# Optimization experiments

Hardware: AMD Instinct MI355X
Metric: run time of the kernel (lower is better)

The kernel has to match this reference:

```python
import jax, jax.numpy as jnp
import numpy as np

UNITS = 256
IN_DIM = 256
OUT_DIM = 10
TOL = 1e-4
MAX_ITER = 50


def setup_inputs() -> dict:
    key = jax.random.key(0)
    ks = jax.random.split(key, 16)
    B = 65536
    s = 1.0 / np.sqrt(UNITS)
    inp = {
        "x": jax.random.normal(ks[0], (B, IN_DIM), dtype=jnp.float32),
        "w_in": jax.random.normal(ks[1], (IN_DIM, UNITS), dtype=jnp.float32) * s,
        "b_in": jax.random.normal(ks[2], (UNITS,), dtype=jnp.float32) * 0.01,
        "w_out": jax.random.normal(ks[3], (UNITS, OUT_DIM), dtype=jnp.float32) * s,
        "b_out": jax.random.normal(ks[4], (OUT_DIM,), dtype=jnp.float32) * 0.01,
    }
    eye = jnp.eye(UNITS, dtype=jnp.float32)
    for i in range(4):
        # well-conditioned (invertible) implicit-layer weight: I + small perturbation
        inp[f"w{i+1}"] = eye + 0.1 * jax.random.normal(ks[5 + 2 * i], (UNITS, UNITS), dtype=jnp.float32) * s
        inp[f"b{i+1}"] = jax.random.normal(ks[6 + 2 * i], (UNITS,), dtype=jnp.float32) * 0.01
    return inp


def newton_block(x, W, b):
    # Solve z @ W = x + tanh(x) + b by Newton iteration with early exit on ||g||.
    c = x + jnp.tanh(x) + b  # [B, n]
    z0 = x
    g0 = z0 @ W - c

    def cond(state):
        z, g, it = state
        return (it < MAX_ITER) & (jnp.linalg.norm(g) >= TOL)

    def body(state):
        z, g, it = state
        # torch.solve(g[:, :, None], W^T.repeat(B,1,1)): shared matrix -> one solve
        z = z - jnp.linalg.solve(W.T, g.T).T
        g = z @ W - c
        return (z, g, it + 1)

    z, _, _ = jax.lax.while_loop(cond, body, (z0, g0, jnp.asarray(0)))
    z = jax.lax.stop_gradient(z)  # torch loop runs under no_grad
    # final differentiable correction (torch: z = z - (z@W - x - tanh(x) - b))
    return z - (z @ W - c)


def reference(x, w_in, b_in, w1, b1, w2, b2, w3, b3, w4, b4, w_out, b_out):
    z = x @ w_in + b_in
    z = newton_block(z, w1, b1)
    z = newton_block(z, w2, b2)
    z = newton_block(z, w3, b3)
    z = newton_block(z, w4, b4)
    logits = z @ w_out + b_out
    return jax.nn.softmax(logits, axis=1)
```

## Files before the change

kernel.cpp:

```cpp
#include <hip/hip_runtime.h>
#include <hip/hip_fp16.h>
#include <math.h>


typedef __attribute__((ext_vector_type(8))) short short8;
typedef __attribute__((ext_vector_type(4))) float f32x4;

__device__ __forceinline__ float tanh_fast(float x) {
#if __has_builtin(__builtin_amdgcn_exp2f)
  float e = __builtin_amdgcn_exp2f(x * 2.8853900817779268f);
#else
  float e = __expf(2.0f * x);
#endif
  return 1.0f - 2.0f * __builtin_amdgcn_rcpf(e + 1.0f);
}
__device__ __forceinline__ unsigned rn_pair16(float v0, float v1) {
  __half2 h = __floats2half2_rn(v0, v1);
  return *reinterpret_cast<unsigned*>(&h);
}
__device__ __forceinline__ unsigned rtz_pair16(float v0, float v1) {
#if __has_builtin(__builtin_amdgcn_cvt_pkrtz)
  typedef __fp16 h2v __attribute__((ext_vector_type(2)));
  h2v h = __builtin_amdgcn_cvt_pkrtz(v0, v1);
  return *reinterpret_cast<unsigned*>(&h);
#else
  return rn_pair16(v0, v1);
#endif
}

__global__ __launch_bounds__(256) void ns_poly_k(
    const float* __restrict__ w1, const float* __restrict__ w2,
    const float* __restrict__ w3, const float* __restrict__ w4,
    const float* __restrict__ w_in, const float* __restrict__ w_out,
    unsigned* __restrict__ pk) {
  const int bid = blockIdx.x;
  const int t = threadIdx.x;
  if (bid >= 256) {
    int idx = (bid - 256) * 256 + t;
    {
      int kc = idx >> 12;
      int nt = (idx >> 8) & 15;
      int lane = (idx >> 2) & 63;
      int d = idx & 3;
      int n = nt * 16 + (lane & 15);
      int kb = kc * 32 + (lane >> 4) * 8 + d * 2;
      pk[idx] = rn_pair16(w_in[kb * 256 + n], w_in[(kb + 1) * 256 + n]);
    }
    int idx2 = idx + 32768;
    if (idx2 < 34816) {
      int r2 = idx2 - 32768;
      int kc = r2 >> 8;
      int lane = (r2 >> 2) & 63;
      int d = r2 & 3;
      int n = lane & 15;
      int kb = kc * 32 + (lane >> 4) * 8 + d * 2;
      float v0 = (n < 10) ? w_out[kb * 10 + n] : 0.0f;
      float v1 = (n < 10) ? w_out[(kb + 1) * 10 + n] : 0.0f;
      pk[5 * 32768 + r2] = rn_pair16(v0, v1);
    }
    return;
  }
  const int m = bid >> 6;
  const int r0 = (bid & 63) * 4;
  const float* __restrict__ W = (m == 0) ? w1 : (m == 1) ? w2 : (m == 2) ? w3 : w4;
  __shared__ float S[4][256];

#pragma unroll
  for (int i = 0; i < 4; ++i) {
    int e = i * 256 + t;
    int r = e >> 8, c = e & 255;
    S[r][c] = (((r0 + r) == c) ? 6.0f : 0.0f) - W[(r0 + r) * 256 + c];
  }
  __syncthreads();

  const float coef[4] = {-15.0f, 20.0f, -15.0f, 6.0f};
#pragma unroll
  for (int step = 0; step < 4; ++step) {
    float acc[4];
#pragma unroll
    for (int r = 0; r < 4; ++r) acc[r] = 0.0f;
    for (int k = 0; k < 256; k += 4) {
      float4 sv[4];
#pragma unroll
      for (int r = 0; r < 4; ++r) sv[r] = *(const float4*)&S[r][k];
      float wv0 = W[(k + 0) * 256 + t];
      float wv1 = W[(k + 1) * 256 + t];
      float wv2 = W[(k + 2) * 256 + t];
      float wv3 = W[(k + 3) * 256 + t];
#pragma unroll
      for (int r = 0; r < 4; ++r) {
        acc[r] = fmaf(sv[r].x, wv0, acc[r]);
        acc[r] = fmaf(sv[r].y, wv1, acc[r]);
        acc[r] = fmaf(sv[r].z, wv2, acc[r]);
        acc[r] = fmaf(sv[r].w, wv3, acc[r]);
      }
    }
    __syncthreads();
    float cdiag = coef[step];
#pragma unroll
    for (int r = 0; r < 4; ++r)
      S[r][t] = acc[r] + (((r0 + r) == t) ? cdiag : 0.0f);
    __syncthreads();
  }

  const int kc = r0 >> 5;
  const int quad = (r0 >> 3) & 3;
  const int d0 = (r0 & 7) >> 1;
#pragma unroll
  for (int i = 0; i < 2; ++i) {
    int q = i * 256 + t;
    int nt = q >> 5;
    int n16 = (q >> 1) & 15;
    int dd = q & 1;
    int n = nt * 16 + n16;
    int lane = quad * 16 + n16;
    unsigned word = rn_pair16(S[2 * dd][n], S[2 * dd + 1][n]);
    pk[(m + 1) * 32768 + kc * 4096 + nt * 256 + lane * 4 + (d0 + dd)] = word;
  }
}

#define M_PHASE(PL)                                                            \
  {                                                                            \
    _Pragma("unroll") for (int mt = 0; mt < 4; ++mt)                           \
      _Pragma("unroll") for (int nt = 0; nt < 4; ++nt)                         \
        acc[mt][nt] = (f32x4){0.f, 0.f, 0.f, 0.f};                             \
    _Pragma("unroll") for (int kc = 0; kc < 8; ++kc) {                         \
      short8 zf[4];                                                            \
      _Pragma("unroll") for (int mt = 0; mt < 4; ++mt) {                       \
        int mm = mt * 16 + n16;                                                \
        zf[mt] = *(const short8*)&(PL)[mm * 256 + (((kc * 4 + quad) ^ (mm & 31)) * 8)]; \
      }                                                                        \
      _Pragma("unroll") for (int mt = 0; mt < 4; ++mt)                         \
        _Pragma("unroll") for (int nt = 0; nt < 4; ++nt)                       \
          acc[mt][nt] = __builtin_amdgcn_mfma_f32_16x16x32_f16(                \
              wreg[nt][kc], zf[mt], acc[mt][nt], 0, 0, 0);                     \
      __builtin_amdgcn_sched_barrier(0);                                       \
    }                                                                          \
  }

#define E_PHASE(PL, BN, BI, DOTANH)                                            \
  {                                                                            \
    _Pragma("unroll") for (int nt = 0; nt < 4; ++nt) {                         \
      int colb = wv * 64 + nt * 16 + quad * 4;                                 \
      float4 bi4 = make_float4(0.f, 0.f, 0.f, 0.f);                            \
      float4 bn4 = make_float4(0.f, 0.f, 0.f, 0.f);                            \
      if ((BI) != nullptr) bi4 = *(const float4*)((BI) + colb);                \
      if (DOTANH) bn4 = *(const float4*)((BN) + colb);                         \
      _Pragma("unroll") for (int mt = 0; mt < 4; ++mt) {                       \
        int row = mt * 16 + n16;                                               \
        float v0 = acc[mt][nt][0] + bi4.x;                                     \
        float v1 = acc[mt][nt][1] + bi4.y;                                     \
        float v2 = acc[mt][nt][2] + bi4.z;                                     \
        float v3 = acc[mt][nt][3] + bi4.w;                                     \
        if (DOTANH) {                                                          \
          v0 = v0 + tanh_fast(v0) + bn4.x;                                     \
          v1 = v1 + tanh_fast(v1) + bn4.y;                                     \
          v2 = v2 + tanh_fast(v2) + bn4.z;                                     \
          v3 = v3 + tanh_fast(v3) + bn4.w;                                     \
        }                                                                      \
        int idx = row * 256 + (((colb >> 3) ^ (row & 31)) * 8) + (colb & 7);   \
        uint2 zp;                                                              \
        zp.x = rtz_pair16(v0, v1);                                             \
        zp.y = rtz_pair16(v2, v3);                                             \
        *(uint2*)&(PL)[idx] = zp;                                              \
      }                                                                        \
    }                                                                          \
  }

#define LOAD_WREG(LAYER)                                                       \
  {                                                                            \
    const unsigned* pkl = pk + (LAYER) * 32768 + wv * 1024 + ln * 4;           \
    _Pragma("unroll") for (int nt = 0; nt < 4; ++nt)                           \
      _Pragma("unroll") for (int kc = 0; kc < 8; ++kc)                         \
        wreg[nt][kc] = *(const short8*)(pkl + kc * 4096 + nt * 256);           \
  }

__global__ __launch_bounds__(256)
__attribute__((amdgpu_waves_per_eu(2, 2)))
void fused3_k(
    const float* __restrict__ x, const unsigned* __restrict__ pk,
    const float* __restrict__ b_in,
    const float* __restrict__ b1, const float* __restrict__ b2,
    const float* __restrict__ b3, const float* __restrict__ b4,
    const float* __restrict__ b_out, float* __restrict__ out) {
  __shared__ unsigned short zpl[2 * 64 * 256];
  const int t = threadIdx.x;
  const int ln = t & 63;
  const int wv = t >> 6;
  const int quad = ln >> 4;
  const int n16 = ln & 15;
  const int grow0 = blockIdx.x * 128;

  short8 wreg[4][8];
  f32x4 acc[4][4];

  LOAD_WREG(0);

#pragma unroll
  for (int i = 0; i < 32; ++i) {
    int e = i * 1024 + t * 4;
    int r = e >> 8, c = e & 255;
    float4 v = *(const float4*)(x + (grow0 + r) * 256 + c);
    int u = r >> 6, rl = r & 63;
    int idx = u * 16384 + rl * 256 + (((c >> 3) ^ (rl & 31)) * 8) + (c & 7);
    uint2 zp;
    zp.x = rtz_pair16(v.x, v.y);
    zp.y = rtz_pair16(v.z, v.w);
    *(uint2*)&zpl[idx] = zp;
  }
  __syncthreads();

  unsigned short* pl0 = zpl;
  unsigned short* pl1 = zpl + 16384;
  const float* bnv[4] = {b1, b2, b3, b4};

  for (int layer = 0; layer < 5; ++layer) {
    const float* bn = (layer < 4) ? bnv[layer] : nullptr;
    const float* bi0 = (layer == 0) ? b_in : nullptr;
    const bool dt = (layer < 4);

    M_PHASE(pl0);
    __syncthreads();
    E_PHASE(pl0, bn, bi0, dt);
    M_PHASE(pl1);
    __syncthreads();
    if (layer < 4) LOAD_WREG(layer + 1);
    E_PHASE(pl1, bn, bi0, dt);
  }
  __syncthreads();

  {
    f32x4 lacc[2][4];
#pragma unroll
    for (int u = 0; u < 2; ++u)
#pragma unroll
      for (int mt = 0; mt < 4; ++mt) lacc[u][mt] = (f32x4){0.f, 0.f, 0.f, 0.f};
    const unsigned* pw = pk + 5 * 32768 + ln * 4;
#pragma unroll
    for (int kk = 0; kk < 2; ++kk) {
      int kc = wv * 2 + kk;
      short8 wh = *(const short8*)(pw + kc * 256);
#pragma unroll
      for (int u = 0; u < 2; ++u) {
        const unsigned short* pl = zpl + u * 16384;
#pragma unroll
        for (int mt = 0; mt < 4; ++mt) {
          int mm = mt * 16 + n16;
          short8 zf = *(const short8*)&pl[mm * 256 + (((kc * 4 + quad) ^ (mm & 31)) * 8)];
          lacc[u][mt] = __builtin_amdgcn_mfma_f32_16x16x32_f16(wh, zf, lacc[u][mt], 0, 0, 0);
        }
      }
    }
    __syncthreads();
#pragma unroll
    for (int u = 0; u < 2; ++u) {
      float* pbuf = (float*)(zpl + u * 16384);
#pragma unroll
      for (int mt = 0; mt < 4; ++mt) {
        int addr = wv * 1024 + (mt * 16 + n16) * 16 + quad * 4;
        *(f32x4*)&pbuf[addr] = lacc[u][mt];
      }
    }
    __syncthreads();
    if (t < 128) {
      int u = t >> 6;
      int rl = t & 63;
      const float* pbuf = (const float*)(zpl + u * 16384);
      float lg[10];
      float mx = -1e30f;
#pragma unroll
      for (int j = 0; j < 10; ++j) {
        float s = b_out[j];
#pragma unroll
        for (int w2 = 0; w2 < 4; ++w2) s += pbuf[w2 * 1024 + rl * 16 + j];
        lg[j] = s;
        mx = fmaxf(mx, s);
      }
      float sum = 0.f;
#pragma unroll
      for (int j = 0; j < 10; ++j) {
        lg[j] = __expf(lg[j] - mx);
        sum += lg[j];
      }
      float inv = 1.0f / sum;
      float* op = out + (grow0 + t) * 10;
#pragma unroll
      for (int j = 0; j < 10; ++j) op[j] = lg[j] * inv;
    }
  }
}

extern "C" void kernel_launch(void* const* d_in, const int* in_sizes, int n_in,
                              void* d_out, int out_size, void* d_ws, size_t ws_size,
                              hipStream_t stream) {
  const float* x     = (const float*)d_in[0];
  const float* w_in  = (const float*)d_in[1];
  const float* b_in  = (const float*)d_in[2];
  const float* w_out = (const float*)d_in[3];
  const float* b_out = (const float*)d_in[4];
  const float* w1 = (const float*)d_in[5];
  const float* b1 = (const float*)d_in[6];
  const float* w2 = (const float*)d_in[7];
  const float* b2 = (const float*)d_in[8];
  const float* w3 = (const float*)d_in[9];
  const float* b3 = (const float*)d_in[10];
  const float* w4 = (const float*)d_in[11];
  const float* b4 = (const float*)d_in[12];
  float* out = (float*)d_out;

  unsigned* pk = (unsigned*)d_ws;

  ns_poly_k<<<384, 256, 0, stream>>>(w1, w2, w3, w4, w_in, w_out, pk);
  fused3_k<<<512, 256, 0, stream>>>(x, pk, b_in, b1, b2, b3, b4, b_out, out);
}
```

Measured before the change: 205.6 us.

## Double-buffer LDS fragment reads in MFMA loop and split inverse-polynomial kernel

The MFMA phase now double-buffers its LDS fragment reads, loading the next k-chunk while the current chunk's MFMAs run, and raises wave priority around the MFMA groups. This is meant to hide LDS latency behind the matrix units. Separately, the weight-inverse polynomial kernel now gives each block 2 rows instead of 4 and launches twice as many blocks, for more parallelism in the preprocessing step. The cost is extra register pressure from the second fragment buffer, and each W element is read from global memory twice as often in preprocessing.

```diff
diff --git a/kernel.cpp b/kernel.cpp
--- a/kernel.cpp
+++ b/kernel.cpp
@@ -35,8 +35,8 @@
     unsigned* __restrict__ pk) {
   const int bid = blockIdx.x;
   const int t = threadIdx.x;
-  if (bid >= 256) {
-    int idx = (bid - 256) * 256 + t;
+  if (bid >= 512) {
+    int idx = (bid - 512) * 256 + t;
     {
       int kc = idx >> 12;
       int nt = (idx >> 8) & 15;
@@ -60,82 +60,83 @@
     }
     return;
   }
-  const int m = bid >> 6;
-  const int r0 = (bid & 63) * 4;
+  const int m = bid >> 7;
+  const int r0 = (bid & 127) * 2;
   const float* __restrict__ W = (m == 0) ? w1 : (m == 1) ? w2 : (m == 2) ? w3 : w4;
-  __shared__ float S[4][256];
-
-#pragma unroll
-  for (int i = 0; i < 4; ++i) {
-    int e = i * 256 + t;
-    int r = e >> 8, c = e & 255;
-    S[r][c] = (((r0 + r) == c) ? 6.0f : 0.0f) - W[(r0 + r) * 256 + c];
-  }
+  __shared__ float S[2][256];
+
+  S[0][t] = ((r0 == t) ? 6.0f : 0.0f) - W[r0 * 256 + t];
+  S[1][t] = (((r0 + 1) == t) ? 6.0f : 0.0f) - W[(r0 + 1) * 256 + t];
   __syncthreads();
 
   const float coef[4] = {-15.0f, 20.0f, -15.0f, 6.0f};
 #pragma unroll
   for (int step = 0; step < 4; ++step) {
-    float acc[4];
-#pragma unroll
-    for (int r = 0; r < 4; ++r) acc[r] = 0.0f;
+    float acc0 = 0.0f, acc1 = 0.0f;
     for (int k = 0; k < 256; k += 4) {
-      float4 sv[4];
-#pragma unroll
-      for (int r = 0; r < 4; ++r) sv[r] = *(const float4*)&S[r][k];
+      float4 sv0 = *(const float4*)&S[0][k];
+      float4 sv1 = *(const float4*)&S[1][k];
       float wv0 = W[(k + 0) * 256 + t];
       float wv1 = W[(k + 1) * 256 + t];
       float wv2 = W[(k + 2) * 256 + t];
       float wv3 = W[(k + 3) * 256 + t];
-#pragma unroll
-      for (int r = 0; r < 4; ++r) {
-        acc[r] = fmaf(sv[r].x, wv0, acc[r]);
-        acc[r] = fmaf(sv[r].y, wv1, acc[r]);
-        acc[r] = fmaf(sv[r].z, wv2, acc[r]);
-        acc[r] = fmaf(sv[r].w, wv3, acc[r]);
-      }
+      acc0 = fmaf(sv0.x, wv0, acc0); acc1 = fmaf(sv1.x, wv0, acc1);
+      acc0 = fmaf(sv0.y, wv1, acc0); acc1 = fmaf(sv1.y, wv1, acc1);
+      acc0 = fmaf(sv0.z, wv2, acc0); acc1 = fmaf(sv1.z, wv2, acc1);
+      acc0 = fmaf(sv0.w, wv3, acc0); acc1 = fmaf(sv1.w, wv3, acc1);
     }
     __syncthreads();
     float cdiag = coef[step];
-#pragma unroll
-    for (int r = 0; r < 4; ++r)
-      S[r][t] = acc[r] + (((r0 + r) == t) ? cdiag : 0.0f);
+    S[0][t] = acc0 + ((r0 == t) ? cdiag : 0.0f);
+    S[1][t] = acc1 + (((r0 + 1) == t) ? cdiag : 0.0f);
     __syncthreads();
   }
 
   const int kc = r0 >> 5;
   const int quad = (r0 >> 3) & 3;
-  const int d0 = (r0 & 7) >> 1;
-#pragma unroll
-  for (int i = 0; i < 2; ++i) {
-    int q = i * 256 + t;
-    int nt = q >> 5;
-    int n16 = (q >> 1) & 15;
-    int dd = q & 1;
-    int n = nt * 16 + n16;
+  const int d = (r0 & 7) >> 1;
+  {
+    int n = t;
+    int nt = n >> 4;
+    int n16 = n & 15;
     int lane = quad * 16 + n16;
-    unsigned word = rn_pair16(S[2 * dd][n], S[2 * dd + 1][n]);
-    pk[(m + 1) * 32768 + kc * 4096 + nt * 256 + lane * 4 + (d0 + dd)] = word;
-  }
-}
-
+    pk[(m + 1) * 32768 + kc * 4096 + nt * 256 + lane * 4 + d] =
+        rn_pair16(S[0][n], S[1][n]);
+  }
+}
+
+#define ZREAD(DST, PL, KC)                                                     \
+  {                                                                            \
+    _Pragma("unroll") for (int mt = 0; mt < 4; ++mt) {                         \
+      int mm = mt * 16 + n16;                                                  \
+      DST[mt] = *(const short8*)&(PL)[mm * 256 + ((((KC) * 4 + quad) ^ (mm & 31)) * 8)]; \
+    }                                                                          \
+  }
+#define ZMMA(SRC, KC)                                                          \
+  {                                                                            \
+    __builtin_amdgcn_s_setprio(1);                                             \
+    _Pragma("unroll") for (int mt = 0; mt < 4; ++mt)                           \
+      _Pragma("unroll") for (int nt = 0; nt < 4; ++nt)                         \
+        acc[mt][nt] = __builtin_amdgcn_mfma_f32_16x16x32_f16(                  \
+            wreg[nt][KC], SRC[mt], acc[mt][nt], 0, 0, 0);                      \
+    __builtin_amdgcn_s_setprio(0);                                             \
+  }
 #define M_PHASE(PL)                                                            \
   {                                                                            \
     _Pragma("unroll") for (int mt = 0; mt < 4; ++mt)                           \
       _Pragma("unroll") for (int nt = 0; nt < 4; ++nt)                         \
         acc[mt][nt] = (f32x4){0.f, 0.f, 0.f, 0.f};                             \
-    _Pragma("unroll") for (int kc = 0; kc < 8; ++kc) {                         \
-      short8 zf[4];                                                            \
-      _Pragma("unroll") for (int mt = 0; mt < 4; ++mt) {                       \
-        int mm = mt * 16 + n16;                                                \
-        zf[mt] = *(const short8*)&(PL)[mm * 256 + (((kc * 4 + quad) ^ (mm & 31)) * 8)]; \
-      }                                                                        \
-      _Pragma("unroll") for (int mt = 0; mt < 4; ++mt)                         \
-        _Pragma("unroll") for (int nt = 0; nt < 4; ++nt)                       \
-          acc[mt][nt] = __builtin_amdgcn_mfma_f32_16x16x32_f16(                \
-              wreg[nt][kc], zf[mt], acc[mt][nt], 0, 0, 0);                     \
-      __builtin_amdgcn_sched_barrier(0);                                       \
-    }                                                                          \
+    short8 zfA[4], zfB[4];                                                     \
+    ZREAD(zfA, PL, 0);                                                         \
+    __builtin_amdgcn_sched_barrier(0);                                         \
+    ZREAD(zfB, PL, 1); ZMMA(zfA, 0); __builtin_amdgcn_sched_barrier(0);        \
+    ZREAD(zfA, PL, 2); ZMMA(zfB, 1); __builtin_amdgcn_sched_barrier(0);        \
+    ZREAD(zfB, PL, 3); ZMMA(zfA, 2); __builtin_amdgcn_sched_barrier(0);        \
+    ZREAD(zfA, PL, 4); ZMMA(zfB, 3); __builtin_amdgcn_sched_barrier(0);        \
+    ZREAD(zfB, PL, 5); ZMMA(zfA, 4); __builtin_amdgcn_sched_barrier(0);        \
+    ZREAD(zfA, PL, 6); ZMMA(zfB, 5); __builtin_amdgcn_sched_barrier(0);        \
+    ZREAD(zfB, PL, 7); ZMMA(zfA, 6); __builtin_amdgcn_sched_barrier(0);        \
+    ZMMA(zfB, 7);                                                              \
   }
 
 #define E_PHASE(PL, BN, BI, DOTANH)                                            \
@@ -310,6 +311,6 @@
 
   unsigned* pk = (unsigned*)d_ws;
 
-  ns_poly_k<<<384, 256, 0, stream>>>(w1, w2, w3, w4, w_in, w_out, pk);
+  ns_poly_k<<<640, 256, 0, stream>>>(w1, w2, w3, w4, w_in, w_out, pk);
   fused3_k<<<512, 256, 0, stream>>>(x, pk, b_in, b1, b2, b3, b4, b_out, out);
 }
```

Measured after the change: 215.6 us. 1.05x slower.

## Split weight registers by K-half and keep both tile accumulators live

Applied to the files above, without the earlier changes.

Weight fragments now live in half-size register arrays loaded in two K-halves per layer, and both 64-row tiles accumulate concurrently in a doubled accumulator array. This replaces the alternating per-tile matmul/epilogue schedule with two matmul passes per K-half followed by a joint epilogue, and adds s_setprio around the MFMA passes. The change trades weight-register pressure for accumulator registers and adds a mid-layer global reload of the second K-half of the weights, which may stall the MFMA pipe. It also drops the overlap between one tile's epilogue and the other tile's matmul.

```diff
diff --git a/kernel.cpp b/kernel.cpp
--- a/kernel.cpp
+++ b/kernel.cpp
@@ -119,27 +119,36 @@
   }
 }
 
-#define M_PHASE(PL)                                                            \
+#define LOAD_W(LAYER, KB)                                                      \
   {                                                                            \
-    _Pragma("unroll") for (int mt = 0; mt < 4; ++mt)                           \
-      _Pragma("unroll") for (int nt = 0; nt < 4; ++nt)                         \
-        acc[mt][nt] = (f32x4){0.f, 0.f, 0.f, 0.f};                             \
-    _Pragma("unroll") for (int kc = 0; kc < 8; ++kc) {                         \
+    const unsigned* pkl = pk + (LAYER) * 32768 + (KB) * 4096 + wv * 1024 + ln * 4; \
+    _Pragma("unroll") for (int j = 0; j < 4; ++j)                              \
+      _Pragma("unroll") for (int k4 = 0; k4 < 4; ++k4)                         \
+        wreg[j][k4] = *(const short8*)(pkl + k4 * 4096 + j * 256);             \
+  }
+
+#define M_PASS(U, KB)                                                          \
+  {                                                                            \
+    const unsigned short* pl = zpl + (U) * 16384;                              \
+    __builtin_amdgcn_s_setprio(1);                                             \
+    _Pragma("unroll") for (int k4 = 0; k4 < 4; ++k4) {                         \
       short8 zf[4];                                                            \
       _Pragma("unroll") for (int mt = 0; mt < 4; ++mt) {                       \
         int mm = mt * 16 + n16;                                                \
-        zf[mt] = *(const short8*)&(PL)[mm * 256 + (((kc * 4 + quad) ^ (mm & 31)) * 8)]; \
+        zf[mt] = *(const short8*)&pl[mm * 256 + (((((KB) + k4) * 4 + quad) ^ (mm & 31)) * 8)]; \
       }                                                                        \
       _Pragma("unroll") for (int mt = 0; mt < 4; ++mt)                         \
         _Pragma("unroll") for (int nt = 0; nt < 4; ++nt)                       \
-          acc[mt][nt] = __builtin_amdgcn_mfma_f32_16x16x32_f16(                \
-              wreg[nt][kc], zf[mt], acc[mt][nt], 0, 0, 0);                     \
-      __builtin_amdgcn_sched_barrier(0);                                       \
+          acc[U][mt][nt] = __builtin_amdgcn_mfma_f32_16x16x32_f16(             \
+              wreg[nt][k4], zf[mt], acc[U][mt][nt], 0, 0, 0);                  \
     }                                                                          \
-  }
-
-#define E_PHASE(PL, BN, BI, DOTANH)                                            \
+    __builtin_amdgcn_s_setprio(0);                                             \
+    __builtin_amdgcn_sched_barrier(0);                                         \
+  }
+
+#define E_TILE(U, BN, BI, DOTANH)                                              \
   {                                                                            \
+    unsigned short* pl = zpl + (U) * 16384;                                    \
     _Pragma("unroll") for (int nt = 0; nt < 4; ++nt) {                         \
       int colb = wv * 64 + nt * 16 + quad * 4;                                 \
       float4 bi4 = make_float4(0.f, 0.f, 0.f, 0.f);                            \
@@ -148,10 +157,10 @@
       if (DOTANH) bn4 = *(const float4*)((BN) + colb);                         \
       _Pragma("unroll") for (int mt = 0; mt < 4; ++mt) {                       \
         int row = mt * 16 + n16;                                               \
-        float v0 = acc[mt][nt][0] + bi4.x;                                     \
-        float v1 = acc[mt][nt][1] + bi4.y;                                     \
-        float v2 = acc[mt][nt][2] + bi4.z;                                     \
-        float v3 = acc[mt][nt][3] + bi4.w;                                     \
+        float v0 = acc[U][mt][nt][0] + bi4.x;                                  \
+        float v1 = acc[U][mt][nt][1] + bi4.y;                                  \
+        float v2 = acc[U][mt][nt][2] + bi4.z;                                  \
+        float v3 = acc[U][mt][nt][3] + bi4.w;                                  \
         if (DOTANH) {                                                          \
           v0 = v0 + tanh_fast(v0) + bn4.x;                                     \
           v1 = v1 + tanh_fast(v1) + bn4.y;                                     \
@@ -162,17 +171,9 @@
         uint2 zp;                                                              \
         zp.x = rtz_pair16(v0, v1);                                             \
         zp.y = rtz_pair16(v2, v3);                                             \
-        *(uint2*)&(PL)[idx] = zp;                                              \
+        *(uint2*)&pl[idx] = zp;                                                \
       }                                                                        \
     }                                                                          \
-  }
-
-#define LOAD_WREG(LAYER)                                                       \
-  {                                                                            \
-    const unsigned* pkl = pk + (LAYER) * 32768 + wv * 1024 + ln * 4;           \
-    _Pragma("unroll") for (int nt = 0; nt < 4; ++nt)                           \
-      _Pragma("unroll") for (int kc = 0; kc < 8; ++kc)                         \
-        wreg[nt][kc] = *(const short8*)(pkl + kc * 4096 + nt * 256);           \
   }
 
 __global__ __launch_bounds__(256)
@@ -191,10 +192,10 @@
   const int n16 = ln & 15;
   const int grow0 = blockIdx.x * 128;
 
-  short8 wreg[4][8];
-  f32x4 acc[4][4];
-
-  LOAD_WREG(0);
+  short8 wreg[4][4];
+  f32x4 acc[2][4][4];
+
+  LOAD_W(0, 0);
 
 #pragma unroll
   for (int i = 0; i < 32; ++i) {
@@ -210,8 +211,6 @@
   }
   __syncthreads();
 
-  unsigned short* pl0 = zpl;
-  unsigned short* pl1 = zpl + 16384;
   const float* bnv[4] = {b1, b2, b3, b4};
 
   for (int layer = 0; layer < 5; ++layer) {
@@ -219,15 +218,24 @@
     const float* bi0 = (layer == 0) ? b_in : nullptr;
     const bool dt = (layer < 4);
 
-    M_PHASE(pl0);
-    __syncthreads();
-    E_PHASE(pl0, bn, bi0, dt);
-    M_PHASE(pl1);
-    __syncthreads();
-    if (layer < 4) LOAD_WREG(layer + 1);
-    E_PHASE(pl1, bn, bi0, dt);
-  }
-  __syncthreads();
+#pragma unroll
+    for (int u = 0; u < 2; ++u)
+#pragma unroll
+      for (int mt = 0; mt < 4; ++mt)
+#pragma unroll
+        for (int nt = 0; nt < 4; ++nt) acc[u][mt][nt] = (f32x4){0.f, 0.f, 0.f, 0.f};
+
+    M_PASS(0, 0);
+    M_PASS(1, 0);
+    LOAD_W(layer, 4);
+    M_PASS(0, 4);
+    M_PASS(1, 4);
+    if (layer < 4) LOAD_W(layer + 1, 0);
+    __syncthreads();
+    E_TILE(0, bn, bi0, dt);
+    E_TILE(1, bn, bi0, dt);
+    __syncthreads();
+  }
 
   {
     f32x4 lacc[2][4];
```

Measured after the change: 207.4 us. No clear change (+0.9%).
